# Optimization experiments

Measured on AMD Instinct MI355X. Metric: run time of the kernel, lower is better.

Reference implementation:

```python
import jax, jax.numpy as jnp
import numpy as np

# 7 axial hex directions (dy, dx) including center, matching HexConv2d.DIRS
DIRS = [(0, 0), (1, 0), (0, 1), (-1, 1), (-1, 0), (0, -1), (1, -1)]


def _shift(x, dy, dx):
    """torch.roll-style shift with zero fill at wrapped edges. x: [B,C,H,W]."""
    sx, sy = -dx, -dy
    y = jnp.roll(x, shift=(sy, sx), axis=(2, 3))
    if sy > 0:
        y = y.at[:, :, :sy, :].set(0)
    elif sy < 0:
        y = y.at[:, :, sy:, :].set(0)
    if sx > 0:
        y = y.at[:, :, :, :sx].set(0)
    elif sx < 0:
        y = y.at[:, :, :, sx:].set(0)
    return y


def _hex_mask(H, dtype):
    size = H // 2
    q = jnp.arange(-size, size + 1)
    Q, R = jnp.meshgrid(q, q, indexing='ij')
    S = -Q - R
    # |Q|<=size and |R|<=size hold by construction; only |S|<=size cuts corners
    mask = ((jnp.abs(Q) <= size) & (jnp.abs(R) <= size) & (jnp.abs(S) <= size))
    return mask.astype(dtype)[None, None]  # [1,1,H,W]


def setup_inputs() -> dict:
    key = jax.random.key(0)
    k1, k2, k3 = jax.random.split(key, 3)
    B, Cin, Cout, H = 32, 256, 256, 49
    x = jax.random.normal(k1, (B, Cin, H, H), dtype=jnp.float32)
    weight = jax.random.normal(k2, (Cout, Cin, 7), dtype=jnp.float32) * 0.02
    bias = jax.random.normal(k3, (Cout,), dtype=jnp.float32) * 0.02
    return {"x": x, "weight": weight, "bias": bias}


def reference(x, weight, bias):
    mask = _hex_mask(x.shape[2], x.dtype)          # [1,1,H,W]
    x = x * mask
    # [7,B,C,H,W]: shifted+masked neighbor maps
    nbr = jnp.stack([_shift(x, dy, dx) for (dy, dx) in DIRS], axis=0) * mask
    # fused 1x1 conv over (channel, direction): weight [O,C,7]
    y = jnp.einsum('nbchw,ocn->bohw', nbr, weight) + bias[None, :, None, None]
    return y * mask
```

## Files before the change

### kernel.cpp

```cpp
#include <hip/hip_runtime.h>


typedef __attribute__((ext_vector_type(8))) short short8;
typedef __attribute__((ext_vector_type(4))) short short4v;
typedef __attribute__((ext_vector_type(4))) float floatx4;

#define NPIX   2401
#define W50    50
#define PREAL  2450
#define XBLEAD 56
#define XBROWS 2672
#define PT12   80
#define NT12   32
#define NSEG12 12
#define BUF12  (NSEG12*1024)
#define XB3_BYTES ((size_t)32*XBROWS*256*2)
#define WP_BYTES  917504ULL
#define WS_NEED3  (XB3_BYTES + WP_BYTES)
#define NPADROW 271

#define X4_BLKS 4864
#define Z_BLKS  1084
#define W_BLKS  224
#define PREP_BLKS (X4_BLKS + Z_BLKS + W_BLKS)

__device__ __forceinline__ unsigned short f2bf(float f) {
  unsigned u = __builtin_bit_cast(unsigned, f);
  u += 0x7fffu + ((u >> 16) & 1u);
  return (unsigned short)(u >> 16);
}

__device__ __forceinline__ void prep_w_body(const float* __restrict__ w,
                                            unsigned short* __restrict__ wp, int tt) {
  int l  = tt & 63;
  int ot = (tt >> 6) & 15;
  int kc = (tt >> 10) & 7;
  int n  = tt >> 13;
  int o  = ot * 16 + (l & 15);
  int cb = kc * 32 + ((l >> 4) * 8);
  const float* src = w + (size_t)(o * 256 + cb) * 7 + n;
  short8 pk;
#pragma unroll
  for (int j = 0; j < 8; ++j) pk[j] = (short)f2bf(src[j * 7]);
  ((short8*)wp)[tt] = pk;
}

__global__ __launch_bounds__(256)
void prep_all(const float* __restrict__ x, const float* __restrict__ w,
              unsigned short* __restrict__ xb, unsigned short* __restrict__ wp) {
  __shared__ unsigned short t[64][68];
  const int tid = threadIdx.x;
  const int blk = blockIdx.x;

  if (blk < X4_BLKS) {
    const int l = blk;
    const int span = l % 38, cg = (l / 38) & 3, b = l / 152;
    const int s0 = span * 64;
    {
      const int chl = tid >> 2, i4 = tid & 3;
      const float* src = x + ((size_t)(b * 256 + cg * 64 + chl)) * NPIX;
      const int rbase = s0 + i4 * 16;
#pragma unroll
      for (int it = 0; it < 4; ++it) {
        int r = rbase + it * 4;
        float vv[4] = {0.f, 0.f, 0.f, 0.f};
        if (r + 3 < NPIX) {
          float4 v = *(const float4*)(src + r);
          vv[0] = v.x; vv[1] = v.y; vv[2] = v.z; vv[3] = v.w;
        } else {
#pragma unroll
          for (int e = 0; e < 4; ++e) if (r + e < NPIX) vv[e] = src[r + e];
        }
        short4v u = {0, 0, 0, 0};
#pragma unroll
        for (int e = 0; e < 4; ++e) {
          int re = r + e;
          unsigned short uu = 0;
          if (re < NPIX) {
            int h = re / 49, ww = re - h * 49, s = h + ww;
            if (s >= 24 && s <= 72) uu = f2bf(vv[e]);
          }
          u[e] = (short)uu;
        }
        *(short4v*)&t[chl][i4 * 16 + it * 4] = u;
      }
    }
    __syncthreads();
    const int pp = tid >> 3;
    const int co = tid & 7;
    unsigned d[8];
#pragma unroll
    for (int k = 0; k < 8; ++k) d[k] = *(const unsigned*)&t[co * 8 + k][pp * 2];
    uint4 lo, hi;
    {
      unsigned l0[4], h0[4];
#pragma unroll
      for (int m = 0; m < 4; ++m) {
        unsigned a = d[2 * m], bq = d[2 * m + 1];
        l0[m] = (a & 0xffffu) | (bq << 16);
        h0[m] = (a >> 16) | (bq & 0xffff0000u);
      }
      lo = make_uint4(l0[0], l0[1], l0[2], l0[3]);
      hi = make_uint4(h0[0], h0[1], h0[2], h0[3]);
    }
    const int r_lo = s0 + pp * 2, r_hi = r_lo + 1;
    if (r_lo < NPIX) {
      int prow = r_lo + r_lo / 49 + XBLEAD;
      *(uint4*)(xb + ((size_t)b * XBROWS + prow) * 256 + cg * 64 + co * 8) = lo;
    }
    if (r_hi < NPIX) {
      int prow = r_hi + r_hi / 49 + XBLEAD;
      *(uint4*)(xb + ((size_t)b * XBROWS + prow) * 256 + cg * 64 + co * 8) = hi;
    }
  } else if (blk < X4_BLKS + Z_BLKS) {
    int idx = (blk - X4_BLKS) * 256 + tid;
    if (idx >= 32 * NPADROW * 32) return;
    int c16 = idx & 31;
    int rr  = idx >> 5;
    int pr  = rr % NPADROW;
    int b   = rr / NPADROW;
    int row;
    if (pr < 56)        row = pr;
    else if (pr < 105)  row = 105 + 50 * (pr - 56);
    else                row = 2506 + (pr - 105);
    short8 z = {0,0,0,0,0,0,0,0};
    *(short8*)(xb + ((size_t)b * XBROWS + row) * 256 + c16 * 8) = z;
  } else {
    prep_w_body(w, wp, (blk - X4_BLKS - Z_BLKS) * 256 + tid);
  }
}

__global__ void prep_w_kernel(const float* __restrict__ w, unsigned short* __restrict__ wp) {
  prep_w_body(w, wp, blockIdx.x * 256 + threadIdx.x);
}

__global__ __launch_bounds__(256, 4)
void hexconv_v12(const unsigned short* __restrict__ xb,
                 const unsigned short* __restrict__ wp,
                 const float* __restrict__ bias,
                 float* __restrict__ out) {
  __shared__ __attribute__((aligned(16))) unsigned char smem[2 * BUF12];

  const int tid  = threadIdx.x;
  const int lane = tid & 63;
  const int wv   = tid >> 6;
  const int col  = lane & 15;
  const int quad = lane >> 4;

  const int bx  = blockIdx.x;
  const int oh  = bx & 1;
  const int bxp = bx >> 1;
  const int pt  = (bxp & 7) * 4 + (bxp >> 3);
  const int b   = blockIdx.y;
  const int P0  = pt * PT12;
  const int phase = (pt + b + oh * 4) & 7;

  const int OFF[7] = {0, 50, 1, -49, -50, -1, 49};

  int ba[7];
#pragma unroll
  for (int n = 0; n < 7; ++n) {
    int r0 = col + 56 + OFF[n];
    int r64 = r0 << 6;
    ba[n] = (r64 + quad * 16) ^ ((r64 >> 3) & 0x30);
  }

  const int gpart = (lane & 3) ^ ((lane >> 3) & 3);
  const char* gsrc0 = (const char*)(xb + ((size_t)b * XBROWS + (size_t)P0) * 256)
                      + (lane >> 2) * 512 + gpart * 16;

  auto stage1 = [&](int buf, int kc) {
    char* ldsb = (char*)smem + buf * BUF12;
    for (int u = wv; u < NSEG12; u += 4) {
      __builtin_amdgcn_global_load_lds(
          (const __attribute__((address_space(1))) unsigned int*)
              (gsrc0 + (size_t)u * 8192 + kc * 64),
          (__attribute__((address_space(3))) unsigned int*)(ldsb + u * 1024), 16, 0, 0);
    }
  };

  const char* wbase = (const char*)wp + (size_t)(oh * 8 + wv * 2) * 1024 + lane * 16;

  floatx4 acc[2][5];
#pragma unroll
  for (int ii = 0; ii < 2; ++ii)
#pragma unroll
    for (int j = 0; j < 5; ++j) acc[ii][j] = (floatx4){0.f, 0.f, 0.f, 0.f};

  stage1(0, phase);
  __syncthreads();

  for (int i = 0; i < 8; ++i) {
    const int kc = (i + phase) & 7;
    if (i < 7) stage1((i + 1) & 1, (i + 1 + phase) & 7);
    const char* bufp = (const char*)smem + (i & 1) * BUF12;
#pragma unroll
    for (int n = 0; n < 7; ++n) {
      short8 af[2];
#pragma unroll
      for (int ii = 0; ii < 2; ++ii)
        af[ii] = *(const short8*)(wbase + ((size_t)((n * 8 + kc) * 16 + ii)) * 1024);
      const char* bp = bufp + ba[n];
      short8 bfv[5];
#pragma unroll
      for (int j = 0; j < 5; ++j)
        bfv[j] = *(const short8*)(bp + j * 1024);
      __builtin_amdgcn_s_setprio(1);
#pragma unroll
      for (int j = 0; j < 5; ++j)
#pragma unroll
        for (int ii = 0; ii < 2; ++ii)
          acc[ii][j] = __builtin_amdgcn_mfma_f32_16x16x32_bf16(af[ii], bfv[j], acc[ii][j], 0, 0, 0);
      __builtin_amdgcn_s_setprio(0);
    }
    if (i < 7) __syncthreads();
  }

  const int ob = oh * 128 + wv * 32;
#pragma unroll
  for (int ii = 0; ii < 2; ++ii) {
    floatx4 bv = *(const floatx4*)(bias + ob + ii * 16 + quad * 4);
#pragma unroll
    for (int j = 0; j < 5; ++j)
#pragma unroll
      for (int rr = 0; rr < 4; ++rr) acc[ii][j][rr] += bv[rr];
  }

#pragma unroll
  for (int j = 0; j < 5; ++j) {
    int p = P0 + j * 16 + col;
    int h = p / W50;
    int w = p - h * W50;
    if (w >= 49 || p >= PREAL) continue;
    bool m = (h + w >= 24) && (h + w <= 72);
    int ridx = h * 49 + w;
#pragma unroll
    for (int ii = 0; ii < 2; ++ii) {
      float* dst = out + ((b * 256 + ob + ii * 16 + quad * 4) * NPIX + ridx);
#pragma unroll
      for (int rr = 0; rr < 4; ++rr) {
        float v = m ? acc[ii][j][rr] : 0.f;
        dst[rr * NPIX] = v;
      }
    }
  }
}

#define PITCH  40
#define V1WIN  168
#define V1ZROW 168
__global__ __launch_bounds__(256)
void hexconv_v1(const float* __restrict__ x,
                const unsigned short* __restrict__ wp,
                const float* __restrict__ bias,
                float* __restrict__ out) {
  __shared__ unsigned short sm[(V1ZROW + 2) * PITCH];
  const int tid = threadIdx.x, lane = tid & 63, wv = tid >> 6;
  const int col = lane & 15, quad = lane >> 4;
  const int pt = blockIdx.x, b = blockIdx.y;
  const int P0 = pt * 64, win_start = P0 - 52;
  if (tid < PITCH * 2) sm[V1ZROW * PITCH + tid] = 0;
  const int OFF[7] = {0, 49, 1, -48, -49, -1, 48};
  const int DXP = (1 << 2) | (1 << 3), DXN = (1 << 5) | (1 << 6);
  int baddr[4][7];
#pragma unroll
  for (int j = 0; j < 4; ++j) {
    int pix = P0 + j * 16 + col;
    int wj = pix % 49;
    int rowbase = pix - win_start;
#pragma unroll
    for (int n = 0; n < 7; ++n) {
      bool bad = (((DXP >> n) & 1) && wj == 48) || (((DXN >> n) & 1) && wj == 0);
      int row = bad ? V1ZROW : (rowbase + OFF[n]);
      baddr[j][n] = row * (PITCH * 2) + quad * 16;
    }
  }
  int sp[3], sgp[3]; bool sok[3];
#pragma unroll
  for (int pi = 0; pi < 3; ++pi) {
    int p = lane + pi * 64, gp = win_start + p;
    sp[pi] = p; sgp[pi] = gp;
    bool hm = false;
    if (gp >= 0 && gp < NPIX) { int h = gp / 49, w = gp - h * 49, s = h + w; hm = (s >= 24 && s <= 72); }
    sok[pi] = (p < V1WIN) && hm;
  }
  floatx4 acc[4][4];
#pragma unroll
  for (int i = 0; i < 4; ++i)
#pragma unroll
    for (int j = 0; j < 4; ++j) acc[i][j] = (floatx4){0.f, 0.f, 0.f, 0.f};
  const short8* wpv = (const short8*)wp;
  const int wslot = wv * 4;
  for (int kc = 0; kc < 8; ++kc) {
    __syncthreads();
#pragma unroll
    for (int ci = 0; ci < 8; ++ci) {
      int c = ci * 4 + wv;
      const float* src = x + ((size_t)(b * 256 + kc * 32 + c)) * NPIX;
#pragma unroll
      for (int pi = 0; pi < 3; ++pi) {
        if (sp[pi] < V1WIN) {
          float v = sok[pi] ? src[sgp[pi]] : 0.f;
          sm[sp[pi] * PITCH + c] = f2bf(v);
        }
      }
    }
    __syncthreads();
#pragma unroll
    for (int n = 0; n < 7; ++n) {
      short8 af[4];
#pragma unroll
      for (int i = 0; i < 4; ++i)
        af[i] = wpv[((size_t)((n * 8 + kc) * 16 + wslot + i)) * 64 + lane];
      short8 bf[4];
#pragma unroll
      for (int j = 0; j < 4; ++j)
        bf[j] = *(const short8*)((const char*)sm + baddr[j][n]);
#pragma unroll
      for (int i = 0; i < 4; ++i)
#pragma unroll
        for (int j = 0; j < 4; ++j)
          acc[i][j] = __builtin_amdgcn_mfma_f32_16x16x32_bf16(af[i], bf[j], acc[i][j], 0, 0, 0);
    }
  }
  const int ob = wv * 64;
  floatx4 bv[4];
#pragma unroll
  for (int i = 0; i < 4; ++i)
    bv[i] = *(const floatx4*)(bias + ob + i * 16 + quad * 4);
#pragma unroll
  for (int j = 0; j < 4; ++j) {
    int pix = P0 + j * 16 + col;
    if (pix >= NPIX) continue;
    int h = pix / 49, w = pix - h * 49;
    bool m = (h + w >= 24 && h + w <= 72);
#pragma unroll
    for (int i = 0; i < 4; ++i) {
      int o = ob + i * 16 + quad * 4;
      float* dst = out + ((size_t)(b * 256 + o)) * NPIX + pix;
#pragma unroll
      for (int r = 0; r < 4; ++r) {
        float v = m ? (acc[i][j][r] + bv[i][r]) : 0.f;
        dst[(size_t)r * NPIX] = v;
      }
    }
  }
}

extern "C" void kernel_launch(void* const* d_in, const int* in_sizes, int n_in,
                              void* d_out, int out_size, void* d_ws, size_t ws_size,
                              hipStream_t stream) {
  const float* x    = (const float*)d_in[0];
  const float* w    = (const float*)d_in[1];
  const float* bias = (const float*)d_in[2];
  float* out = (float*)d_out;

  if (ws_size >= WS_NEED3) {
    unsigned short* xb = (unsigned short*)d_ws;
    unsigned short* wp = (unsigned short*)((char*)d_ws + XB3_BYTES);
    prep_all<<<PREP_BLKS, 256, 0, stream>>>(x, w, xb, wp);
    hexconv_v12<<<dim3(64, 32), 256, 0, stream>>>(xb, wp, bias, out);
  } else {
    unsigned short* wp = (unsigned short*)d_ws;
    prep_w_kernel<<<224, 256, 0, stream>>>(w, wp);
    hexconv_v1<<<dim3(38, 32), 256, 0, stream>>>(x, wp, bias, out);
  }
}
```

Measured before the change: 236.9 us.

## Switch hex conv to 32x32x16 MFMA with larger tiles and triple-buffered LDS

Replaces the 16x16x32 MFMA kernel with a 32x32x16 variant in which each block covers all 256 output channels and 160 pixels, so the grid shrinks from 64x32 to 16x32 blocks. The x tile is triple-buffered in LDS, weight fragments are register-prefetched one step ahead, and the weight prep layout is reordered to match the new fragment shape. The goal is better MFMA throughput and more reuse of each staged x tile across output channels. In exchange it uses far more accumulator registers and LDS, lowers occupancy to 2 blocks per CU, and leaves only 512 blocks, which may load-balance unevenly across CUs.

```diff
diff --git a/kernel.cpp b/kernel.cpp
--- a/kernel.cpp
+++ b/kernel.cpp
@@ -1,19 +1,19 @@
 #include <hip/hip_runtime.h>
 
 
-typedef __attribute__((ext_vector_type(8))) short short8;
-typedef __attribute__((ext_vector_type(4))) short short4v;
-typedef __attribute__((ext_vector_type(4))) float floatx4;
+typedef __attribute__((ext_vector_type(8)))  short short8;
+typedef __attribute__((ext_vector_type(4)))  short short4v;
+typedef __attribute__((ext_vector_type(4)))  float floatx4;
+typedef __attribute__((ext_vector_type(16))) float floatx16;
 
 #define NPIX   2401
 #define W50    50
 #define PREAL  2450
 #define XBLEAD 56
 #define XBROWS 2672
-#define PT12   80
-#define NT12   32
-#define NSEG12 12
-#define BUF12  (NSEG12*1024)
+#define PT14   160
+#define NSEG14 17
+#define SLOT14 (NSEG14*1024)
 #define XB3_BYTES ((size_t)32*XBROWS*256*2)
 #define WP_BYTES  917504ULL
 #define WS_NEED3  (XB3_BYTES + WP_BYTES)
@@ -39,6 +39,21 @@
   int o  = ot * 16 + (l & 15);
   int cb = kc * 32 + ((l >> 4) * 8);
   const float* src = w + (size_t)(o * 256 + cb) * 7 + n;
+  short8 pk;
+#pragma unroll
+  for (int j = 0; j < 8; ++j) pk[j] = (short)f2bf(src[j * 7]);
+  ((short8*)wp)[tt] = pk;
+}
+
+__device__ __forceinline__ void prep_w2_body(const float* __restrict__ w,
+                                             unsigned short* __restrict__ wp, int tt) {
+  int l   = tt & 63;
+  int ot2 = (tt >> 6) & 7;
+  int g   = (tt >> 9) & 15;
+  int n   = tt >> 13;
+  int o   = ot2 * 32 + (l & 31);
+  int c0  = g * 16 + ((l >> 5) * 8);
+  const float* src = w + (size_t)(o * 256 + c0) * 7 + n;
   short8 pk;
 #pragma unroll
   for (int j = 0; j < 8; ++j) pk[j] = (short)f2bf(src[j * 7]);
@@ -126,7 +141,7 @@
     short8 z = {0,0,0,0,0,0,0,0};
     *(short8*)(xb + ((size_t)b * XBROWS + row) * 256 + c16 * 8) = z;
   } else {
-    prep_w_body(w, wp, (blk - X4_BLKS - Z_BLKS) * 256 + tid);
+    prep_w2_body(w, wp, (blk - X4_BLKS - Z_BLKS) * 256 + tid);
   }
 }
 
@@ -134,44 +149,40 @@
   prep_w_body(w, wp, blockIdx.x * 256 + threadIdx.x);
 }
 
-__global__ __launch_bounds__(256, 4)
-void hexconv_v12(const unsigned short* __restrict__ xb,
+__global__ __launch_bounds__(256, 2)
+void hexconv_v14(const unsigned short* __restrict__ xb,
                  const unsigned short* __restrict__ wp,
                  const float* __restrict__ bias,
                  float* __restrict__ out) {
-  __shared__ __attribute__((aligned(16))) unsigned char smem[2 * BUF12];
-
-  const int tid  = threadIdx.x;
-  const int lane = tid & 63;
-  const int wv   = tid >> 6;
-  const int col  = lane & 15;
-  const int quad = lane >> 4;
-
-  const int bx  = blockIdx.x;
-  const int oh  = bx & 1;
-  const int bxp = bx >> 1;
-  const int pt  = (bxp & 7) * 4 + (bxp >> 3);
-  const int b   = blockIdx.y;
-  const int P0  = pt * PT12;
-  const int phase = (pt + b + oh * 4) & 7;
+  __shared__ __attribute__((aligned(16))) unsigned char smem[3 * SLOT14];
+
+  const int tid   = threadIdx.x;
+  const int lane  = tid & 63;
+  const int wv    = tid >> 6;
+  const int col32 = lane & 31;
+  const int hi    = lane >> 5;
+
+  const int pt = blockIdx.x;
+  const int b  = blockIdx.y;
+  const int P0 = pt * PT14;
+  const int phase = (pt + b) & 7;
 
   const int OFF[7] = {0, 50, 1, -49, -50, -1, 49};
 
   int ba[7];
 #pragma unroll
   for (int n = 0; n < 7; ++n) {
-    int r0 = col + 56 + OFF[n];
-    int r64 = r0 << 6;
-    ba[n] = (r64 + quad * 16) ^ ((r64 >> 3) & 0x30);
+    int rn = col32 + 56 + OFF[n];
+    ba[n] = rn * 64 + ((hi ^ ((rn >> 1) & 1)) << 4) + (((rn >> 2) & 1) << 5);
   }
 
   const int gpart = (lane & 3) ^ ((lane >> 3) & 3);
   const char* gsrc0 = (const char*)(xb + ((size_t)b * XBROWS + (size_t)P0) * 256)
                       + (lane >> 2) * 512 + gpart * 16;
 
-  auto stage1 = [&](int buf, int kc) {
-    char* ldsb = (char*)smem + buf * BUF12;
-    for (int u = wv; u < NSEG12; u += 4) {
+  auto stage1 = [&](int slot, int kc) {
+    char* ldsb = (char*)smem + slot * SLOT14;
+    for (int u = wv; u < NSEG14; u += 4) {
       __builtin_amdgcn_global_load_lds(
           (const __attribute__((address_space(1))) unsigned int*)
               (gsrc0 + (size_t)u * 8192 + kc * 64),
@@ -179,68 +190,94 @@
     }
   };
 
-  const char* wbase = (const char*)wp + (size_t)(oh * 8 + wv * 2) * 1024 + lane * 16;
-
-  floatx4 acc[2][5];
-#pragma unroll
-  for (int ii = 0; ii < 2; ++ii)
-#pragma unroll
-    for (int j = 0; j < 5; ++j) acc[ii][j] = (floatx4){0.f, 0.f, 0.f, 0.f};
+  const char* wbA = (const char*)wp + (size_t)(wv * 2) * 1024 + lane * 16;
+
+  short8 afr[2][2];
+  floatx16 acc[2][5];
+#pragma unroll
+  for (int t = 0; t < 2; ++t)
+#pragma unroll
+    for (int j = 0; j < 5; ++j)
+#pragma unroll
+      for (int e = 0; e < 16; ++e) acc[t][j][e] = 0.f;
 
   stage1(0, phase);
+  stage1(1, (1 + phase) & 7);
+#pragma unroll
+  for (int t = 0; t < 2; ++t)
+    afr[0][t] = *(const short8*)(wbA + (size_t)((phase * 2) * 8 + t) * 1024);
   __syncthreads();
 
+#pragma unroll 1
   for (int i = 0; i < 8; ++i) {
-    const int kc = (i + phase) & 7;
-    if (i < 7) stage1((i + 1) & 1, (i + 1 + phase) & 7);
-    const char* bufp = (const char*)smem + (i & 1) * BUF12;
-#pragma unroll
-    for (int n = 0; n < 7; ++n) {
-      short8 af[2];
-#pragma unroll
-      for (int ii = 0; ii < 2; ++ii)
-        af[ii] = *(const short8*)(wbase + ((size_t)((n * 8 + kc) * 16 + ii)) * 1024);
-      const char* bp = bufp + ba[n];
+    const int ci  = (i + phase) & 7;
+    const int cin = (i + 1 + phase) & 7;
+    if (i < 6) stage1((i + 2) % 3, (i + 2 + phase) & 7);
+    const char* slotp = (const char*)smem + (i % 3) * SLOT14;
+#pragma unroll
+    for (int s = 0; s < 14; ++s) {
+      const int n   = s >> 1;
+      const int kk2 = s & 1;
+      const int cs  = s & 1;
+      const int ns  = cs ^ 1;
+      if (s < 13) {
+        const int n2 = (s + 1) >> 1;
+        const int g2 = ci * 2 + ((s + 1) & 1);
+#pragma unroll
+        for (int t = 0; t < 2; ++t)
+          afr[ns][t] = *(const short8*)(wbA + (size_t)((n2 * 16 + g2) * 8 + t) * 1024);
+      } else if (i < 7) {
+        const int g2 = cin * 2;
+#pragma unroll
+        for (int t = 0; t < 2; ++t)
+          afr[ns][t] = *(const short8*)(wbA + (size_t)(g2 * 8 + t) * 1024);
+      }
+      const char* bp = slotp + (ba[n] ^ (kk2 << 5));
       short8 bfv[5];
 #pragma unroll
+      for (int j = 0; j < 5; ++j) bfv[j] = *(const short8*)(bp + j * 2048);
+      __builtin_amdgcn_s_setprio(1);
+#pragma unroll
       for (int j = 0; j < 5; ++j)
-        bfv[j] = *(const short8*)(bp + j * 1024);
-      __builtin_amdgcn_s_setprio(1);
+#pragma unroll
+        for (int t = 0; t < 2; ++t)
+          acc[t][j] = __builtin_amdgcn_mfma_f32_32x32x16_bf16(afr[cs][t], bfv[j], acc[t][j], 0, 0, 0);
+      __builtin_amdgcn_s_setprio(0);
+    }
+    __syncthreads();
+  }
+
+#pragma unroll
+  for (int t = 0; t < 2; ++t) {
+#pragma unroll
+    for (int g4 = 0; g4 < 4; ++g4) {
+      floatx4 bv = *(const floatx4*)(bias + wv * 64 + t * 32 + g4 * 8 + hi * 4);
 #pragma unroll
       for (int j = 0; j < 5; ++j)
 #pragma unroll
-        for (int ii = 0; ii < 2; ++ii)
-          acc[ii][j] = __builtin_amdgcn_mfma_f32_16x16x32_bf16(af[ii], bfv[j], acc[ii][j], 0, 0, 0);
-      __builtin_amdgcn_s_setprio(0);
-    }
-    if (i < 7) __syncthreads();
-  }
-
-  const int ob = oh * 128 + wv * 32;
-#pragma unroll
-  for (int ii = 0; ii < 2; ++ii) {
-    floatx4 bv = *(const floatx4*)(bias + ob + ii * 16 + quad * 4);
-#pragma unroll
-    for (int j = 0; j < 5; ++j)
-#pragma unroll
-      for (int rr = 0; rr < 4; ++rr) acc[ii][j][rr] += bv[rr];
+        for (int e = 0; e < 4; ++e) acc[t][j][g4 * 4 + e] += bv[e];
+    }
   }
 
 #pragma unroll
   for (int j = 0; j < 5; ++j) {
-    int p = P0 + j * 16 + col;
+    int p = P0 + j * 32 + col32;
     int h = p / W50;
     int w = p - h * W50;
     if (w >= 49 || p >= PREAL) continue;
     bool m = (h + w >= 24) && (h + w <= 72);
     int ridx = h * 49 + w;
 #pragma unroll
-    for (int ii = 0; ii < 2; ++ii) {
-      float* dst = out + ((b * 256 + ob + ii * 16 + quad * 4) * NPIX + ridx);
-#pragma unroll
-      for (int rr = 0; rr < 4; ++rr) {
-        float v = m ? acc[ii][j][rr] : 0.f;
-        dst[rr * NPIX] = v;
+    for (int t = 0; t < 2; ++t) {
+#pragma unroll
+      for (int g4 = 0; g4 < 4; ++g4) {
+        int och0 = wv * 64 + t * 32 + g4 * 8 + hi * 4;
+        float* dst = out + ((b * 256 + och0) * NPIX + ridx);
+#pragma unroll
+        for (int e = 0; e < 4; ++e) {
+          float v = m ? acc[t][j][g4 * 4 + e] : 0.f;
+          dst[e * NPIX] = v;
+        }
       }
     }
   }
@@ -359,7 +396,7 @@
     unsigned short* xb = (unsigned short*)d_ws;
     unsigned short* wp = (unsigned short*)((char*)d_ws + XB3_BYTES);
     prep_all<<<PREP_BLKS, 256, 0, stream>>>(x, w, xb, wp);
-    hexconv_v12<<<dim3(64, 32), 256, 0, stream>>>(xb, wp, bias, out);
+    hexconv_v14<<<dim3(16, 32), 256, 0, stream>>>(xb, wp, bias, out);
   } else {
     unsigned short* wp = (unsigned short*)d_ws;
     prep_w_kernel<<<224, 256, 0, stream>>>(w, wp);
```

Measured after the change: 234.0 us. No clear change (-1.2%).
